# Performance work log

Hardware: AMD Instinct MI355X
Metric: run time of the kernel (lower is better)

Reference implementation:

```python
import jax, jax.numpy as jnp
import numpy as np

N_NODES = 100000
N_EDGES = 3200000
N_GRAPHS = 128
IN_DIM = 4
HID = 64
BN_EPS = 1e-5


def setup_inputs() -> dict:
    key = jax.random.key(0)
    ks = jax.random.split(key, 24)
    x = jax.random.normal(ks[0], (N_NODES, IN_DIM), dtype=jnp.float32)
    edge_index = jax.random.randint(ks[1], (2, N_EDGES), 0, N_NODES, dtype=jnp.int32)
    batch_ids = jnp.sort(jax.random.randint(ks[2], (N_NODES,), 0, N_GRAPHS, dtype=jnp.int32))

    def lin(k, out_d, in_d):
        s = 1.0 / np.sqrt(in_d)
        return jax.random.uniform(k, (out_d, in_d), jnp.float32, -s, s)

    inp = {
        'x': x, 'edge_index': edge_index, 'batch_ids': batch_ids,
        # SAGEConv i: out = lin_l(mean_neighbors) + lin_r(x_self); bias lives in lin_l
        'w1l': lin(ks[3], HID, IN_DIM), 'b1': jnp.zeros((HID,), jnp.float32), 'w1r': lin(ks[4], HID, IN_DIM),
        'bn1_g': jnp.ones((HID,), jnp.float32), 'bn1_b': jnp.zeros((HID,), jnp.float32),
        'w2l': lin(ks[5], HID, HID), 'b2': jnp.zeros((HID,), jnp.float32), 'w2r': lin(ks[6], HID, HID),
        'bn2_g': jnp.ones((HID,), jnp.float32), 'bn2_b': jnp.zeros((HID,), jnp.float32),
        'w3l': lin(ks[7], HID, HID), 'b3': jnp.zeros((HID,), jnp.float32), 'w3r': lin(ks[8], HID, HID),
        'bn3_g': jnp.ones((HID,), jnp.float32), 'bn3_b': jnp.zeros((HID,), jnp.float32),
        'fc1_w': lin(ks[9], 64, HID), 'fc1_b': jnp.zeros((64,), jnp.float32),
        'fc2_w': lin(ks[10], 2, 64), 'fc2_b': jnp.zeros((2,), jnp.float32),
    }
    return inp


def _sage(x, src, dst, deg_inv, wl, bl, wr):
    # mean-aggregate neighbor messages (source -> target), then two small GEMMs
    msum = jax.ops.segment_sum(x[src], dst, num_segments=N_NODES)  # [N, d]
    agg = msum * deg_inv[:, None]
    return agg @ wl.T + bl + x @ wr.T


def _bn(x, g, b):
    # BatchNorm1d in training mode: batch stats over node dim, biased variance
    m = jnp.mean(x, axis=0)
    v = jnp.mean((x - m) ** 2, axis=0)
    return (x - m) * jax.lax.rsqrt(v + BN_EPS) * g + b


def reference(x, edge_index, batch_ids,
              w1l, b1, w1r, bn1_g, bn1_b,
              w2l, b2, w2r, bn2_g, bn2_b,
              w3l, b3, w3r, bn3_g, bn3_b,
              fc1_w, fc1_b, fc2_w, fc2_b):
    src, dst = edge_index[0], edge_index[1]
    deg = jax.ops.segment_sum(jnp.ones((src.shape[0],), x.dtype), dst, num_segments=N_NODES)
    deg_inv = 1.0 / jnp.maximum(deg, 1.0)

    h = jax.nn.relu(_bn(_sage(x, src, dst, deg_inv, w1l, b1, w1r), bn1_g, bn1_b))
    h = jax.nn.relu(_bn(_sage(h, src, dst, deg_inv, w2l, b2, w2r), bn2_g, bn2_b))
    h = jax.nn.relu(_bn(_sage(h, src, dst, deg_inv, w3l, b3, w3r), bn3_g, bn3_b))

    # global_mean_pool over graphs
    gsum = jax.ops.segment_sum(h, batch_ids, num_segments=N_GRAPHS)
    gcnt = jax.ops.segment_sum(jnp.ones((h.shape[0],), h.dtype), batch_ids, num_segments=N_GRAPHS)
    pooled = gsum / jnp.maximum(gcnt, 1.0)[:, None]

    # MLP head (dropout = identity at inference)
    hid = jax.nn.relu(pooled @ fc1_w.T + fc1_b)
    return hid @ fc2_w.T + fc2_b
```

## Files before the change

### kernel.cpp

```cpp
#include <hip/hip_runtime.h>
#include <hip/hip_fp16.h>

#define NN 100000
#define NE 3200000
#define NG 128
#define BN_EPS 1e-5f

#define NBUK 782
#define BSHIFT 7
#define BCAP 6144

#define GRID_SG 1024
#define PBMAX 2048
#define PSLICE 8

typedef _Float16 h2v __attribute__((ext_vector_type(2)));
typedef unsigned int u32x2 __attribute__((ext_vector_type(2)));
typedef unsigned int u32x4 __attribute__((ext_vector_type(4)));


__global__ void __launch_bounds__(512) k_scatter(
    const int* __restrict__ src, const int* __restrict__ dst,
    int* __restrict__ slab_cursor, unsigned int* __restrict__ slab, int E) {
    __shared__ int hist[NBUK + 2];
    __shared__ int cbase[NBUK + 2];
    int tid = threadIdx.x;
    int eBeg = blockIdx.x * 12500;
    int eEnd = min(eBeg + 12500, E);

    for (int t = tid; t < NBUK; t += 512) hist[t] = 0;
    __syncthreads();
    for (int e = eBeg + tid; e < eEnd; e += 512) {
        int b = dst[e] >> BSHIFT;
        atomicAdd(&hist[b], 1);
    }
    __syncthreads();
    for (int t = tid; t < NBUK; t += 512) {
        int c = hist[t];
        cbase[t] = (c > 0) ? atomicAdd(&slab_cursor[t], c) : 0;
    }
    __syncthreads();
    for (int t = tid; t < NBUK; t += 512) hist[t] = 0;
    __syncthreads();
    for (int e = eBeg + tid; e < eEnd; e += 512) {
        int d = dst[e];
        int b = d >> BSHIFT;
        int r = atomicAdd(&hist[b], 1);
        int pos = cbase[b] + r;
        if (pos < BCAP) slab[(size_t)b * BCAP + pos] = ((unsigned)src[e] << BSHIFT) | (unsigned)(d & 127);
    }
}

__global__ void __launch_bounds__(512) k_bucket_csr(
    const unsigned int* __restrict__ slab, const int* __restrict__ slab_cursor,
    int* __restrict__ row_ptr,
    float* __restrict__ deg_inv, int* __restrict__ csr_src,
    const float* __restrict__ x, const float* __restrict__ w1l,
    const float* __restrict__ b1, const float* __restrict__ w1r,
    __half* __restrict__ hp16, float* __restrict__ part) {
    __shared__ int lds_csr[BCAP];
    __shared__ int red[512];
    __shared__ int sdeg[128];
    __shared__ int sscan[128];
    __shared__ int slcur[128];
    __shared__ float swl[256], swr[256], sb1[64];
    __shared__ float ssum[64], ssq[64];
    int tid = threadIdx.x;
    int b = blockIdx.x;
    int lo = b << BSHIFT;
    int cnt = min(slab_cursor[b], BCAP);
    const unsigned int* sl = slab + (size_t)b * BCAP;

    int partial = 0;
    for (int j = tid; j < b; j += 512) partial += min(slab_cursor[j], BCAP);
    red[tid] = partial;
    __syncthreads();
    for (int off = 256; off > 0; off >>= 1) {
        if (tid < off) red[tid] += red[tid + off];
        __syncthreads();
    }
    int base = red[0];
    if (b == NBUK - 1 && tid == 0) row_ptr[NN] = base + cnt;

    if (tid < 256) { swl[tid] = w1l[tid]; swr[tid] = w1r[tid]; }
    if (tid < 64)  { sb1[tid] = b1[tid]; ssum[tid] = 0.f; ssq[tid] = 0.f; }
    if (tid < 128) sdeg[tid] = 0;
    __syncthreads();

    unsigned int myv[12];
    int mycount = 0;
    for (int k = tid; k < cnt; k += 512) myv[mycount++] = sl[k];
#pragma unroll
    for (int j = 0; j < 12; j++)
        if (j < mycount) atomicAdd(&sdeg[myv[j] & 127], 1);
    __syncthreads();
    int v = (tid < 128) ? sdeg[tid] : 0;
    if (tid < 128) sscan[tid] = v;
    __syncthreads();
    for (int off = 1; off < 128; off <<= 1) {
        int add = 0;
        if (tid < 128 && tid >= off) add = sscan[tid - off];
        __syncthreads();
        if (tid < 128) sscan[tid] += add;
        __syncthreads();
    }
    if (tid < 128) {
        int excl = sscan[tid] - v;
        int n = lo + tid;
        if (n < NN) {
            row_ptr[n] = base + excl;
            deg_inv[n] = 1.0f / fmaxf((float)v, 1.0f);
        }
        slcur[tid] = excl;
    }
    __syncthreads();
#pragma unroll
    for (int j = 0; j < 12; j++)
        if (j < mycount) {
            unsigned int p = myv[j];
            int pos = atomicAdd(&slcur[p & 127], 1);
            lds_csr[pos] = (int)(p >> BSHIFT);
        }
    __syncthreads();
    for (int k = tid; k < cnt; k += 512) csr_src[base + k] = lds_csr[k];

    int i = tid >> 2, c = tid & 3;
    int n = lo + i;
    bool valid = (n < NN);
    int dhi = sscan[i];
    int dlo = dhi - sdeg[i];
    const float4* x4 = (const float4*)x;
    float4 acc = make_float4(0.f, 0.f, 0.f, 0.f);
    int k = dlo + c;
    for (; k + 12 < dhi; k += 16) {
        int s0 = lds_csr[k], s1 = lds_csr[k + 4], s2 = lds_csr[k + 8], s3 = lds_csr[k + 12];
        float4 v0 = x4[s0];
        float4 v1 = x4[s1];
        float4 v2 = x4[s2];
        float4 v3 = x4[s3];
        acc.x += v0.x + v1.x + v2.x + v3.x;
        acc.y += v0.y + v1.y + v2.y + v3.y;
        acc.z += v0.z + v1.z + v2.z + v3.z;
        acc.w += v0.w + v1.w + v2.w + v3.w;
    }
    for (; k < dhi; k += 4) {
        int s = lds_csr[k];
        float4 xv = x4[s];
        acc.x += xv.x; acc.y += xv.y; acc.z += xv.z; acc.w += xv.w;
    }
#pragma unroll
    for (int m = 1; m <= 2; m <<= 1) {
        acc.x += __shfl_xor(acc.x, m);
        acc.y += __shfl_xor(acc.y, m);
        acc.z += __shfl_xor(acc.z, m);
        acc.w += __shfl_xor(acc.w, m);
    }
    float dv = 1.0f / fmaxf((float)sdeg[i], 1.0f);
    float ax = acc.x * dv, ay = acc.y * dv, az = acc.z * dv, aw = acc.w * dv;
    float4 xs = valid ? x4[n] : make_float4(0.f, 0.f, 0.f, 0.f);

#pragma unroll
    for (int m4 = 0; m4 < 4; m4++) {
        float4 o = make_float4(0.f, 0.f, 0.f, 0.f);
        float* op = &o.x;
        if (valid) {
#pragma unroll
            for (int t = 0; t < 4; t++) {
                int j = c * 16 + m4 * 4 + t;
                float s = sb1[j];
                s += ax * swl[j * 4 + 0] + ay * swl[j * 4 + 1] + az * swl[j * 4 + 2] + aw * swl[j * 4 + 3];
                s += xs.x * swr[j * 4 + 0] + xs.y * swr[j * 4 + 1] + xs.z * swr[j * 4 + 2] + xs.w * swr[j * 4 + 3];
                op[t] = s;
            }
            h2v p0 = h2v{(_Float16)o.x, (_Float16)o.y};
            h2v p1 = h2v{(_Float16)o.z, (_Float16)o.w};
            u32x2 w;
            w.x = *(unsigned int*)&p0;
            w.y = *(unsigned int*)&p1;
            __builtin_nontemporal_store(w, (u32x2*)hp16 + (size_t)n * 16 + c * 4 + m4);
        }
        float4 q = make_float4(o.x * o.x, o.y * o.y, o.z * o.z, o.w * o.w);
#pragma unroll
        for (int m = 4; m <= 32; m <<= 1) {
            o.x += __shfl_xor(o.x, m); o.y += __shfl_xor(o.y, m);
            o.z += __shfl_xor(o.z, m); o.w += __shfl_xor(o.w, m);
            q.x += __shfl_xor(q.x, m); q.y += __shfl_xor(q.y, m);
            q.z += __shfl_xor(q.z, m); q.w += __shfl_xor(q.w, m);
        }
        if ((tid & 63) < 4) {
            int jb = c * 16 + m4 * 4;
            atomicAdd(&ssum[jb + 0], o.x); atomicAdd(&ssum[jb + 1], o.y);
            atomicAdd(&ssum[jb + 2], o.z); atomicAdd(&ssum[jb + 3], o.w);
            atomicAdd(&ssq[jb + 0], q.x);  atomicAdd(&ssq[jb + 1], q.y);
            atomicAdd(&ssq[jb + 2], q.z);  atomicAdd(&ssq[jb + 3], q.w);
        }
    }
    __syncthreads();
    if (tid < 64) {
        part[(2 * tid) * PBMAX + blockIdx.x]     = ssum[tid];
        part[(2 * tid + 1) * PBMAX + blockIdx.x] = ssq[tid];
    }
}

__global__ void __launch_bounds__(512, 8) k_sage(
    const __half* __restrict__ h_in, const float* __restrict__ sbv_in,
    const int* __restrict__ row_ptr,
    const int* __restrict__ csr_src, const float* __restrict__ deg_inv,
    const float* __restrict__ wl, const float* __restrict__ bl,
    const float* __restrict__ wr, __half* __restrict__ hp16,
    float* __restrict__ part) {
    __shared__ h2v wl2s[32][68];
    __shared__ h2v wr2s[32][68];
    __shared__ h2v tAh[32][36];
    __shared__ h2v tXh[32][36];
    __shared__ float ssum[64], ssq[64];
    int tid = threadIdx.x;
    for (int idx = tid; idx < 2048; idx += 512) {
        int j = idx & 63, kk = idx >> 6;
        float2 l = ((const float2*)wl)[j * 32 + kk];
        float2 r = ((const float2*)wr)[j * 32 + kk];
        wl2s[kk][j] = h2v{(_Float16)l.x, (_Float16)l.y};
        wr2s[kk][j] = h2v{(_Float16)r.x, (_Float16)r.y};
    }
    if (tid < 64) { ssum[tid] = 0.f; ssq[tid] = 0.f; }
    __syncthreads();

    int g = tid & 15, ni = tid >> 4;
    h2v sch0 = h2v{(_Float16)sbv_in[4 * g + 0], (_Float16)sbv_in[4 * g + 1]};
    h2v sch1 = h2v{(_Float16)sbv_in[4 * g + 2], (_Float16)sbv_in[4 * g + 3]};
    h2v bih0 = h2v{(_Float16)sbv_in[64 + 4 * g + 0], (_Float16)sbv_in[64 + 4 * g + 1]};
    h2v bih1 = h2v{(_Float16)sbv_in[64 + 4 * g + 2], (_Float16)sbv_in[64 + 4 * g + 3]};
    h2v hz = h2v{(_Float16)0.f, (_Float16)0.f};

    const uint2* tbl = (const uint2*)h_in;
    const int ntiles = NN / 32;

#define BN_ACC_H(vv) { \
        h2v a0 = *(h2v*)&vv.x, a1 = *(h2v*)&vv.y; \
        hacc0 += __builtin_elementwise_max(a0 * sch0 + bih0, hz); \
        hacc1 += __builtin_elementwise_max(a1 * sch1 + bih1, hz); }

    for (int tile = blockIdx.x; tile < ntiles; tile += GRID_SG) {
        int n = tile * 32 + ni;
        float ax = 0.f, ay = 0.f, az = 0.f, aw = 0.f;
        int r0 = row_ptr[n], r1 = row_ptr[n + 1];
        int e = r0;
        for (; e + 8 <= r1; e += 8) {
            int s0 = csr_src[e],     s1 = csr_src[e + 1], s2 = csr_src[e + 2], s3 = csr_src[e + 3];
            int s4 = csr_src[e + 4], s5 = csr_src[e + 5], s6 = csr_src[e + 6], s7 = csr_src[e + 7];
            uint2 v0 = tbl[(size_t)s0 * 16 + g];
            uint2 v1 = tbl[(size_t)s1 * 16 + g];
            uint2 v2 = tbl[(size_t)s2 * 16 + g];
            uint2 v3 = tbl[(size_t)s3 * 16 + g];
            uint2 v4 = tbl[(size_t)s4 * 16 + g];
            uint2 v5 = tbl[(size_t)s5 * 16 + g];
            uint2 v6 = tbl[(size_t)s6 * 16 + g];
            uint2 v7 = tbl[(size_t)s7 * 16 + g];
            h2v hacc0 = hz, hacc1 = hz;
            BN_ACC_H(v0) BN_ACC_H(v1) BN_ACC_H(v2) BN_ACC_H(v3)
            BN_ACC_H(v4) BN_ACC_H(v5) BN_ACC_H(v6) BN_ACC_H(v7)
            ax += (float)hacc0.x; ay += (float)hacc0.y;
            az += (float)hacc1.x; aw += (float)hacc1.y;
        }
        for (; e < r1; ++e) {
            int s = csr_src[e];
            uint2 vv = tbl[(size_t)s * 16 + g];
            h2v a0 = *(h2v*)&vv.x, a1 = *(h2v*)&vv.y;
            a0 = __builtin_elementwise_max(a0 * sch0 + bih0, hz);
            a1 = __builtin_elementwise_max(a1 * sch1 + bih1, hz);
            ax += (float)a0.x; ay += (float)a0.y; az += (float)a1.x; aw += (float)a1.y;
        }
        float di = deg_inv[n];
        uint2 rsv = tbl[(size_t)n * 16 + g];
        h2v xs0h = __builtin_elementwise_max(*(h2v*)&rsv.x * sch0 + bih0, hz);
        h2v xs1h = __builtin_elementwise_max(*(h2v*)&rsv.y * sch1 + bih1, hz);
        ax *= di; ay *= di; az *= di; aw *= di;
        tAh[ni][2 * g]     = h2v{(_Float16)ax, (_Float16)ay};
        tAh[ni][2 * g + 1] = h2v{(_Float16)az, (_Float16)aw};
        tXh[ni][2 * g]     = xs0h;
        tXh[ni][2 * g + 1] = xs1h;
        __syncthreads();

        float4 o = ((const float4*)bl)[g];
#pragma unroll 4
        for (int kk = 0; kk < 32; kk++) {
            h2v a2 = tAh[ni][kk];
            h2v x2 = tXh[ni][kk];
            h2v l0 = wl2s[kk][4 * g + 0], l1 = wl2s[kk][4 * g + 1];
            h2v l2 = wl2s[kk][4 * g + 2], l3 = wl2s[kk][4 * g + 3];
            h2v r0v = wr2s[kk][4 * g + 0], r1v = wr2s[kk][4 * g + 1];
            h2v r2v = wr2s[kk][4 * g + 2], r3v = wr2s[kk][4 * g + 3];
#if __has_builtin(__builtin_amdgcn_fdot2)
            o.x = __builtin_amdgcn_fdot2(a2, l0, o.x, false);
            o.y = __builtin_amdgcn_fdot2(a2, l1, o.y, false);
            o.z = __builtin_amdgcn_fdot2(a2, l2, o.z, false);
            o.w = __builtin_amdgcn_fdot2(a2, l3, o.w, false);
            o.x = __builtin_amdgcn_fdot2(x2, r0v, o.x, false);
            o.y = __builtin_amdgcn_fdot2(x2, r1v, o.y, false);
            o.z = __builtin_amdgcn_fdot2(x2, r2v, o.z, false);
            o.w = __builtin_amdgcn_fdot2(x2, r3v, o.w, false);
#else
            float b0 = (float)a2.x, b1 = (float)a2.y, x0 = (float)x2.x, x1 = (float)x2.y;
            o.x += b0 * (float)l0.x + b1 * (float)l0.y + x0 * (float)r0v.x + x1 * (float)r0v.y;
            o.y += b0 * (float)l1.x + b1 * (float)l1.y + x0 * (float)r1v.x + x1 * (float)r1v.y;
            o.z += b0 * (float)l2.x + b1 * (float)l2.y + x0 * (float)r2v.x + x1 * (float)r2v.y;
            o.w += b0 * (float)l3.x + b1 * (float)l3.y + x0 * (float)r3v.x + x1 * (float)r3v.y;
#endif
        }
        {
            h2v p0 = h2v{(_Float16)o.x, (_Float16)o.y};
            h2v p1 = h2v{(_Float16)o.z, (_Float16)o.w};
            u32x2 w;
            w.x = *(unsigned int*)&p0;
            w.y = *(unsigned int*)&p1;
            __builtin_nontemporal_store(w, (u32x2*)hp16 + (size_t)n * 16 + g);
        }

        float4 qv = make_float4(o.x * o.x, o.y * o.y, o.z * o.z, o.w * o.w);
#pragma unroll
        for (int m = 16; m <= 32; m <<= 1) {
            o.x += __shfl_xor(o.x, m); o.y += __shfl_xor(o.y, m);
            o.z += __shfl_xor(o.z, m); o.w += __shfl_xor(o.w, m);
            qv.x += __shfl_xor(qv.x, m); qv.y += __shfl_xor(qv.y, m);
            qv.z += __shfl_xor(qv.z, m); qv.w += __shfl_xor(qv.w, m);
        }
        if ((tid & 48) == 0) {
            atomicAdd(&ssum[4 * g + 0], o.x); atomicAdd(&ssum[4 * g + 1], o.y);
            atomicAdd(&ssum[4 * g + 2], o.z); atomicAdd(&ssum[4 * g + 3], o.w);
            atomicAdd(&ssq[4 * g + 0], qv.x);  atomicAdd(&ssq[4 * g + 1], qv.y);
            atomicAdd(&ssq[4 * g + 2], qv.z);  atomicAdd(&ssq[4 * g + 3], qv.w);
        }
        __syncthreads();
    }
#undef BN_ACC_H
    if (tid < 64) {
        part[(2 * tid) * PBMAX + blockIdx.x]     = ssum[tid];
        part[(2 * tid + 1) * PBMAX + blockIdx.x] = ssq[tid];
    }
}

__global__ void k_reduce_sb(const float* __restrict__ part, int PB,
                            const float* __restrict__ gamma, const float* __restrict__ beta,
                            float* __restrict__ sbv, int N) {
    int c = blockIdx.x;
    float s = 0.f, q = 0.f;
    for (int b = threadIdx.x; b < PB; b += 256) {
        s += part[(2 * c) * PBMAX + b];
        q += part[(2 * c + 1) * PBMAX + b];
    }
    __shared__ float rs[256], rq[256];
    rs[threadIdx.x] = s;
    rq[threadIdx.x] = q;
    __syncthreads();
    for (int off = 128; off > 0; off >>= 1) {
        if (threadIdx.x < off) {
            rs[threadIdx.x] += rs[threadIdx.x + off];
            rq[threadIdx.x] += rq[threadIdx.x + off];
        }
        __syncthreads();
    }
    if (threadIdx.x == 0) {
        float m = rs[0] / (float)N;
        float var = rq[0] / (float)N - m * m;
        float sc = gamma[c] * rsqrtf(var + BN_EPS);
        sbv[c]      = sc;
        sbv[64 + c] = beta[c] - m * sc;
    }
}

__global__ void __launch_bounds__(256) k_pool_partial(
    const __half* __restrict__ hp16, const float* __restrict__ sbv,
    const int* __restrict__ batch, float* __restrict__ pooled_part, int N) {
    __shared__ float ssc[64], sbi[64];
    __shared__ float sm[256];
    if (threadIdx.x < 64) {
        ssc[threadIdx.x] = sbv[threadIdx.x];
        sbi[threadIdx.x] = sbv[64 + threadIdx.x];
    }
    __syncthreads();
    int gph = blockIdx.x >> 3;
    int slice = blockIdx.x & 7;
    int lo = 0, hi = N;
    while (lo < hi) { int mid = (lo + hi) >> 1; if (batch[mid] < gph) lo = mid + 1; else hi = mid; }
    int start = lo;
    hi = N;
    while (lo < hi) { int mid = (lo + hi) >> 1; if (batch[mid] < gph + 1) lo = mid + 1; else hi = mid; }
    int end = lo;

    int c = threadIdx.x & 63, w = threadIdx.x >> 6;
    float s = 0.f;
    for (int r = start + slice * 4 + w; r < end; r += 32)
        s += fmaxf(__half2float(hp16[(size_t)r * 64 + c]) * ssc[c] + sbi[c], 0.f);
    sm[threadIdx.x] = s;
    __syncthreads();
    if (threadIdx.x < 64) {
        float t = sm[c] + sm[64 + c] + sm[128 + c] + sm[192 + c];
        pooled_part[(size_t)(gph * PSLICE + slice) * 64 + c] = t;
    }
}

__global__ void __launch_bounds__(64) k_head(
    const float* __restrict__ pooled_part, const int* __restrict__ batch,
    const float* __restrict__ fc1w, const float* __restrict__ fc1b,
    const float* __restrict__ fc2w, const float* __restrict__ fc2b,
    float* __restrict__ out, int N) {
    __shared__ float pl[64], hid[64];
    int gph = blockIdx.x;
    int j = threadIdx.x;
    int lo = 0, hi = N;
    while (lo < hi) { int mid = (lo + hi) >> 1; if (batch[mid] < gph) lo = mid + 1; else hi = mid; }
    int start = lo;
    hi = N;
    while (lo < hi) { int mid = (lo + hi) >> 1; if (batch[mid] < gph + 1) lo = mid + 1; else hi = mid; }
    int cnt = lo - start;

    float t = 0.f;
#pragma unroll
    for (int s = 0; s < PSLICE; s++) t += pooled_part[(size_t)(gph * PSLICE + s) * 64 + j];
    pl[j] = t / fmaxf((float)cnt, 1.0f);
    __syncthreads();
    float v = fc1b[j];
    for (int k = 0; k < 64; k++) v += pl[k] * fc1w[j * 64 + k];
    hid[j] = fmaxf(v, 0.f);
    __syncthreads();
    if (j < 2) {
        float o = fc2b[j];
        for (int k = 0; k < 64; k++) o += hid[k] * fc2w[j * 64 + k];
        out[gph * 2 + j] = o;
    }
}

extern "C" void kernel_launch(void* const* d_in, const int* in_sizes, int n_in,
                              void* d_out, int out_size, void* d_ws, size_t ws_size,
                              hipStream_t stream) {
    const float* x    = (const float*)d_in[0];
    const int* ei     = (const int*)d_in[1];
    const int* batch  = (const int*)d_in[2];
    const float* w1l  = (const float*)d_in[3];
    const float* b1   = (const float*)d_in[4];
    const float* w1r  = (const float*)d_in[5];
    const float* bn1g = (const float*)d_in[6];
    const float* bn1b = (const float*)d_in[7];
    const float* w2l  = (const float*)d_in[8];
    const float* b2   = (const float*)d_in[9];
    const float* w2r  = (const float*)d_in[10];
    const float* bn2g = (const float*)d_in[11];
    const float* bn2b = (const float*)d_in[12];
    const float* w3l  = (const float*)d_in[13];
    const float* b3   = (const float*)d_in[14];
    const float* w3r  = (const float*)d_in[15];
    const float* bn3g = (const float*)d_in[16];
    const float* bn3b = (const float*)d_in[17];
    const float* fc1w = (const float*)d_in[18];
    const float* fc1b = (const float*)d_in[19];
    const float* fc2w = (const float*)d_in[20];
    const float* fc2b = (const float*)d_in[21];
    float* out = (float*)d_out;

    const int N = NN, E = NE;
    const int* srcp = ei;
    const int* dstp = ei + E;

    char* ws = (char*)d_ws;
    size_t off = 0;
    auto alloc = [&](size_t bytes) -> char* {
        char* p = ws + off;
        off += (bytes + 255) & ~(size_t)255;
        return p;
    };
    int* csr_src       = (int*)alloc(sizeof(int) * E);
    __half* hpA        = (__half*)alloc(sizeof(__half) * N * 64);
    __half* hpB        = (__half*)alloc(sizeof(__half) * N * 64);
    unsigned int* slab = (unsigned int*)alloc(sizeof(unsigned int) * (size_t)NBUK * BCAP);
    int* slab_cursor   = (int*)alloc(sizeof(int) * NBUK);
    int* row_ptr       = (int*)alloc(sizeof(int) * (N + 1));
    float* deg_inv     = (float*)alloc(sizeof(float) * N);
    float* part        = (float*)alloc(sizeof(float) * 128 * PBMAX);
    float* sbv         = (float*)alloc(sizeof(float) * 128);
    float* pooled_part = (float*)alloc(sizeof(float) * NG * PSLICE * 64);

    hipMemsetAsync(slab_cursor, 0, sizeof(int) * NBUK, stream);

    k_scatter<<<256, 512, 0, stream>>>(srcp, dstp, slab_cursor, slab, E);
    k_bucket_csr<<<NBUK, 512, 0, stream>>>(slab, slab_cursor, row_ptr, deg_inv,
                                           csr_src, x, w1l, b1, w1r, hpA, part);
    k_reduce_sb<<<64, 256, 0, stream>>>(part, NBUK, bn1g, bn1b, sbv, N);

    k_sage<<<GRID_SG, 512, 0, stream>>>(hpA, sbv, row_ptr, csr_src, deg_inv,
                                        w2l, b2, w2r, hpB, part);
    k_reduce_sb<<<64, 256, 0, stream>>>(part, GRID_SG, bn2g, bn2b, sbv, N);

    k_sage<<<GRID_SG, 512, 0, stream>>>(hpB, sbv, row_ptr, csr_src, deg_inv,
                                        w3l, b3, w3r, hpA, part);
    k_reduce_sb<<<64, 256, 0, stream>>>(part, GRID_SG, bn3g, bn3b, sbv, N);

    k_pool_partial<<<NG * PSLICE, 256, 0, stream>>>(hpA, sbv, batch, pooled_part, N);
    k_head<<<NG, 64, 0, stream>>>(pooled_part, batch, fc1w, fc1b, fc2w, fc2b, out, N);
}
```

Before: 377.1 us.

## Assign one wavefront per node in SAGE layer with lane-split edge gather

Restructures the SAGE kernel so each 64-lane wavefront handles one node: four lane groups split the neighbor list and reduce with shuffles, then each lane computes one output channel of the dense transform. This removes the block-wide __syncthreads per 32-node tile and the per-tile shared-memory atomics, accumulating BN statistics in registers until the end. The trade-offs are that low-degree nodes leave lanes idle, each lane's output store is only 2 bytes, and the LDS tile handoff now relies on intra-wavefront lockstep without a barrier.

```diff
diff --git a/kernel.cpp b/kernel.cpp
--- a/kernel.cpp
+++ b/kernel.cpp
@@ -211,8 +211,8 @@
     float* __restrict__ part) {
     __shared__ h2v wl2s[32][68];
     __shared__ h2v wr2s[32][68];
-    __shared__ h2v tAh[32][36];
-    __shared__ h2v tXh[32][36];
+    __shared__ h2v tA[8][32];
+    __shared__ h2v tX[8][32];
     __shared__ float ssum[64], ssq[64];
     int tid = threadIdx.x;
     for (int idx = tid; idx < 2048; idx += 512) {
@@ -225,29 +225,31 @@
     if (tid < 64) { ssum[tid] = 0.f; ssq[tid] = 0.f; }
     __syncthreads();
 
-    int g = tid & 15, ni = tid >> 4;
+    int lane = tid & 63, wv = tid >> 6;
+    int g = lane & 15, eo = lane >> 4;
     h2v sch0 = h2v{(_Float16)sbv_in[4 * g + 0], (_Float16)sbv_in[4 * g + 1]};
     h2v sch1 = h2v{(_Float16)sbv_in[4 * g + 2], (_Float16)sbv_in[4 * g + 3]};
     h2v bih0 = h2v{(_Float16)sbv_in[64 + 4 * g + 0], (_Float16)sbv_in[64 + 4 * g + 1]};
     h2v bih1 = h2v{(_Float16)sbv_in[64 + 4 * g + 2], (_Float16)sbv_in[64 + 4 * g + 3]};
     h2v hz = h2v{(_Float16)0.f, (_Float16)0.f};
+    float blj = bl[lane];
+    float lsum = 0.f, lsq = 0.f;
 
     const uint2* tbl = (const uint2*)h_in;
-    const int ntiles = NN / 32;
+    int gw = blockIdx.x * 8 + wv;
 
 #define BN_ACC_H(vv) { \
         h2v a0 = *(h2v*)&vv.x, a1 = *(h2v*)&vv.y; \
         hacc0 += __builtin_elementwise_max(a0 * sch0 + bih0, hz); \
         hacc1 += __builtin_elementwise_max(a1 * sch1 + bih1, hz); }
 
-    for (int tile = blockIdx.x; tile < ntiles; tile += GRID_SG) {
-        int n = tile * 32 + ni;
+    for (int n = gw; n < NN; n += GRID_SG * 8) {
+        int r0 = row_ptr[n], r1 = row_ptr[n + 1];
         float ax = 0.f, ay = 0.f, az = 0.f, aw = 0.f;
-        int r0 = row_ptr[n], r1 = row_ptr[n + 1];
-        int e = r0;
-        for (; e + 8 <= r1; e += 8) {
-            int s0 = csr_src[e],     s1 = csr_src[e + 1], s2 = csr_src[e + 2], s3 = csr_src[e + 3];
-            int s4 = csr_src[e + 4], s5 = csr_src[e + 5], s6 = csr_src[e + 6], s7 = csr_src[e + 7];
+        int e = r0 + eo;
+        for (; e + 28 < r1; e += 32) {
+            int s0 = csr_src[e],      s1 = csr_src[e + 4],  s2 = csr_src[e + 8],  s3 = csr_src[e + 12];
+            int s4 = csr_src[e + 16], s5 = csr_src[e + 20], s6 = csr_src[e + 24], s7 = csr_src[e + 28];
             uint2 v0 = tbl[(size_t)s0 * 16 + g];
             uint2 v1 = tbl[(size_t)s1 * 16 + g];
             uint2 v2 = tbl[(size_t)s2 * 16 + g];
@@ -262,7 +264,7 @@
             ax += (float)hacc0.x; ay += (float)hacc0.y;
             az += (float)hacc1.x; aw += (float)hacc1.y;
         }
-        for (; e < r1; ++e) {
+        for (; e < r1; e += 4) {
             int s = csr_src[e];
             uint2 vv = tbl[(size_t)s * 16 + g];
             h2v a0 = *(h2v*)&vv.x, a1 = *(h2v*)&vv.y;
@@ -270,69 +272,43 @@
             a1 = __builtin_elementwise_max(a1 * sch1 + bih1, hz);
             ax += (float)a0.x; ay += (float)a0.y; az += (float)a1.x; aw += (float)a1.y;
         }
+        ax += __shfl_xor(ax, 16); ax += __shfl_xor(ax, 32);
+        ay += __shfl_xor(ay, 16); ay += __shfl_xor(ay, 32);
+        az += __shfl_xor(az, 16); az += __shfl_xor(az, 32);
+        aw += __shfl_xor(aw, 16); aw += __shfl_xor(aw, 32);
         float di = deg_inv[n];
-        uint2 rsv = tbl[(size_t)n * 16 + g];
-        h2v xs0h = __builtin_elementwise_max(*(h2v*)&rsv.x * sch0 + bih0, hz);
-        h2v xs1h = __builtin_elementwise_max(*(h2v*)&rsv.y * sch1 + bih1, hz);
-        ax *= di; ay *= di; az *= di; aw *= di;
-        tAh[ni][2 * g]     = h2v{(_Float16)ax, (_Float16)ay};
-        tAh[ni][2 * g + 1] = h2v{(_Float16)az, (_Float16)aw};
-        tXh[ni][2 * g]     = xs0h;
-        tXh[ni][2 * g + 1] = xs1h;
-        __syncthreads();
-
-        float4 o = ((const float4*)bl)[g];
+        if (eo == 0) {
+            uint2 rsv = tbl[(size_t)n * 16 + g];
+            h2v xs0h = __builtin_elementwise_max(*(h2v*)&rsv.x * sch0 + bih0, hz);
+            h2v xs1h = __builtin_elementwise_max(*(h2v*)&rsv.y * sch1 + bih1, hz);
+            float bx = ax * di, by = ay * di, bz = az * di, bw = aw * di;
+            tA[wv][2 * g]     = h2v{(_Float16)bx, (_Float16)by};
+            tA[wv][2 * g + 1] = h2v{(_Float16)bz, (_Float16)bw};
+            tX[wv][2 * g]     = xs0h;
+            tX[wv][2 * g + 1] = xs1h;
+        }
+        float o = blj;
 #pragma unroll 4
         for (int kk = 0; kk < 32; kk++) {
-            h2v a2 = tAh[ni][kk];
-            h2v x2 = tXh[ni][kk];
-            h2v l0 = wl2s[kk][4 * g + 0], l1 = wl2s[kk][4 * g + 1];
-            h2v l2 = wl2s[kk][4 * g + 2], l3 = wl2s[kk][4 * g + 3];
-            h2v r0v = wr2s[kk][4 * g + 0], r1v = wr2s[kk][4 * g + 1];
-            h2v r2v = wr2s[kk][4 * g + 2], r3v = wr2s[kk][4 * g + 3];
+            h2v a2 = tA[wv][kk];
+            h2v x2 = tX[wv][kk];
 #if __has_builtin(__builtin_amdgcn_fdot2)
-            o.x = __builtin_amdgcn_fdot2(a2, l0, o.x, false);
-            o.y = __builtin_amdgcn_fdot2(a2, l1, o.y, false);
-            o.z = __builtin_amdgcn_fdot2(a2, l2, o.z, false);
-            o.w = __builtin_amdgcn_fdot2(a2, l3, o.w, false);
-            o.x = __builtin_amdgcn_fdot2(x2, r0v, o.x, false);
-            o.y = __builtin_amdgcn_fdot2(x2, r1v, o.y, false);
-            o.z = __builtin_amdgcn_fdot2(x2, r2v, o.z, false);
-            o.w = __builtin_amdgcn_fdot2(x2, r3v, o.w, false);
+            o = __builtin_amdgcn_fdot2(a2, wl2s[kk][lane], o, false);
+            o = __builtin_amdgcn_fdot2(x2, wr2s[kk][lane], o, false);
 #else
-            float b0 = (float)a2.x, b1 = (float)a2.y, x0 = (float)x2.x, x1 = (float)x2.y;
-            o.x += b0 * (float)l0.x + b1 * (float)l0.y + x0 * (float)r0v.x + x1 * (float)r0v.y;
-            o.y += b0 * (float)l1.x + b1 * (float)l1.y + x0 * (float)r1v.x + x1 * (float)r1v.y;
-            o.z += b0 * (float)l2.x + b1 * (float)l2.y + x0 * (float)r2v.x + x1 * (float)r2v.y;
-            o.w += b0 * (float)l3.x + b1 * (float)l3.y + x0 * (float)r3v.x + x1 * (float)r3v.y;
+            h2v lw = wl2s[kk][lane], rw = wr2s[kk][lane];
+            o += (float)a2.x * (float)lw.x + (float)a2.y * (float)lw.y;
+            o += (float)x2.x * (float)rw.x + (float)x2.y * (float)rw.y;
 #endif
         }
-        {
-            h2v p0 = h2v{(_Float16)o.x, (_Float16)o.y};
-            h2v p1 = h2v{(_Float16)o.z, (_Float16)o.w};
-            u32x2 w;
-            w.x = *(unsigned int*)&p0;
-            w.y = *(unsigned int*)&p1;
-            __builtin_nontemporal_store(w, (u32x2*)hp16 + (size_t)n * 16 + g);
-        }
-
-        float4 qv = make_float4(o.x * o.x, o.y * o.y, o.z * o.z, o.w * o.w);
-#pragma unroll
-        for (int m = 16; m <= 32; m <<= 1) {
-            o.x += __shfl_xor(o.x, m); o.y += __shfl_xor(o.y, m);
-            o.z += __shfl_xor(o.z, m); o.w += __shfl_xor(o.w, m);
-            qv.x += __shfl_xor(qv.x, m); qv.y += __shfl_xor(qv.y, m);
-            qv.z += __shfl_xor(qv.z, m); qv.w += __shfl_xor(qv.w, m);
-        }
-        if ((tid & 48) == 0) {
-            atomicAdd(&ssum[4 * g + 0], o.x); atomicAdd(&ssum[4 * g + 1], o.y);
-            atomicAdd(&ssum[4 * g + 2], o.z); atomicAdd(&ssum[4 * g + 3], o.w);
-            atomicAdd(&ssq[4 * g + 0], qv.x);  atomicAdd(&ssq[4 * g + 1], qv.y);
-            atomicAdd(&ssq[4 * g + 2], qv.z);  atomicAdd(&ssq[4 * g + 3], qv.w);
-        }
-        __syncthreads();
+        __builtin_nontemporal_store((_Float16)o, (_Float16*)hp16 + (size_t)n * 64 + lane);
+        lsum += o;
+        lsq += o * o;
     }
 #undef BN_ACC_H
+    atomicAdd(&ssum[lane], lsum);
+    atomicAdd(&ssq[lane], lsq);
+    __syncthreads();
     if (tid < 64) {
         part[(2 * tid) * PBMAX + blockIdx.x]     = ssum[tid];
         part[(2 * tid + 1) * PBMAX + blockIdx.x] = ssq[tid];
```

Result: slower. 414.1 us (+9.8%).
